# Performance work log

Hardware: AMD Instinct MI355X
Metric: run time of the kernel (lower is better)

## Reference

```python
import jax, jax.numpy as jnp
import numpy as np

T, B, N1, N2, N3, N4 = 512, 256, 512, 256, 64, 784
BETA_LIF = 0.9
BETA_LI = 0.95
THR = 1.0
LN_EPS = 1e-5


@jax.custom_vjp
def spike(x):
    # snntorch heaviside fire with ATan surrogate gradient (alpha=2 default)
    return (x > 0).astype(x.dtype)

def _spike_fwd(x):
    return spike(x), x

def _spike_bwd(x, g):
    return (g / (1.0 + (jnp.pi * x) ** 2),)

spike.defvjp(_spike_fwd, _spike_bwd)


def setup_inputs() -> dict:
    key = jax.random.key(0)
    ks = jax.random.split(key, 10)
    def lin(k, out_d, in_d):
        k1, k2 = jax.random.split(k)
        bound = 1.0 / np.sqrt(in_d)
        W = jax.random.uniform(k1, (out_d, in_d), jnp.float32, -bound, bound)
        b = jax.random.uniform(k2, (out_d,), jnp.float32, -bound, bound)
        return W, b
    W_lif, b_lif = lin(ks[0], N1, N2)
    W_li, b_li = lin(ks[1], N2, N1)
    W1, b1 = lin(ks[2], N3, N2)
    W2, b2 = lin(ks[3], N4, N3)
    # binary spike train input
    spk_rec = (jax.random.uniform(ks[4], (T, B, N2)) < 0.1).astype(jnp.float32)
    return {
        'spk_rec': spk_rec,
        'W_lif': W_lif, 'b_lif': b_lif,
        'W_li': W_li, 'b_li': b_li,
        'W1': W1, 'b1': b1,
        'W2': W2, 'b2': b2,
        'ln_g': jnp.ones((N4,), jnp.float32),
        'ln_b': jnp.zeros((N4,), jnp.float32),
    }


def reference(spk_rec, W_lif, b_lif, W_li, b_li, W1, b1, W2, b2, ln_g, ln_b):
    # Precompute per-step input currents with one big GEMM: [T,B,n1]
    cur_seq = jnp.einsum('tbi,oi->tbo', spk_rec, W_lif) + b_lif

    def lif_step(mem, cur):
        # snntorch Leaky, reset_mechanism='subtract':
        # reset based on previous-step membrane (detached)
        reset = jax.lax.stop_gradient((mem - THR > 0).astype(mem.dtype))
        mem_new = BETA_LIF * mem + cur - reset * THR
        spk = spike(mem_new - THR)
        return mem_new, spk

    mem0 = jnp.zeros(cur_seq.shape[1:], cur_seq.dtype)
    _, lif_spk = jax.lax.scan(lif_step, mem0, cur_seq)  # [T,B,n1]

    li_in = jnp.einsum('tbi,oi->tbo', lif_spk, W_li) + b_li  # [T,B,n2]
    beta_li = jnp.clip(jnp.asarray(BETA_LI, li_in.dtype), 0.0, 1.0)

    def li_step(mem, inp):
        mem = beta_li * mem + inp
        return mem, mem

    _, li_mem = jax.lax.scan(li_step, jnp.zeros(li_in.shape[1:], li_in.dtype), li_in)

    x = li_mem.mean(axis=0)  # [B,n2]
    h = jax.nn.relu(x @ W1.T + b1)  # [B,n3]
    y = h @ W2.T + b2  # [B,n4]
    mu = jnp.mean(y, axis=-1, keepdims=True)
    var = jnp.var(y, axis=-1, keepdims=True)
    return (y - mu) / jnp.sqrt(var + LN_EPS) * ln_g + ln_b
```

## Files before the change

### kernel.cpp

```cpp
#include <hip/hip_runtime.h>
#include <hip/hip_bf16.h>
#include <cmath>
#include <cstdint>


#define T_TOT 512
#define B_SZ  256
#define N1    512
#define N2    256
#define N3    64
#define N4    784
#define BN    (B_SZ * N1)

typedef unsigned short u16;
typedef short bf16x8 __attribute__((ext_vector_type(8)));
typedef float f32x4 __attribute__((ext_vector_type(4)));
typedef const __attribute__((address_space(1))) uint32_t* gas_p;
typedef __attribute__((address_space(3))) uint32_t* las_p;

#define OFF_BLIF 0
#define OFF_WLI  512
#define OFF_BLI  131584
#define OFF_W1   131840
#define OFF_B1   148224
#define OFF_W2   148288
#define OFF_B2   198464
#define OFF_LNG  199248
#define OFF_LNB  200032
#define CANON_N  200816

__device__ __forceinline__ float b2f(u16 u) {
  return __uint_as_float(((uint32_t)u) << 16);
}
__device__ __forceinline__ u16 f2b(float f) {
  uint32_t x = __float_as_uint(f);
  return (u16)((x + 0x7fffu + ((x >> 16) & 1u)) >> 16);
}
__device__ __forceinline__ float ldany(const void* p, long i, int isbf) {
  return isbf ? b2f(((const u16*)p)[i]) : ((const float*)p)[i];
}
__device__ __forceinline__ uint32_t pk_trunc(float a, float b) {
  return (__float_as_uint(a) >> 16) | (__float_as_uint(b) & 0xFFFF0000u);
}

__device__ __forceinline__ void dmax(uint32_t w, uint32_t& mB, uint32_t& mF) {
  uint32_t f = w & 0x7FFFFFFFu; if (f > mF) mF = f;
  uint32_t h0 = (w << 16) & 0x7FFFFFFFu;
  uint32_t h1 = w & 0x7FFF0000u;
  if (h0 > mB) mB = h0;
  if (h1 > mB) mB = h1;
}

__global__ __launch_bounds__(256) void k_prep(
    const void* wA, const void* wB,
    const void* t0, const void* t1, const void* t2,
    const void* s_blif, const void* s_bli, const void* s_w1,
    const void* s_b1, const void* s_w2, const void* spk,
    float* __restrict__ canon, u16* __restrict__ Whi, u16* __restrict__ Wlo,
    uint32_t* __restrict__ flg)
{
  __shared__ uint32_t redA[256], redB[256];
  __shared__ uint32_t dres[12];
  int tid = threadIdx.x;

  #define TREDUCE(vA, vB, oA, oB) {                                          \
    redA[tid] = (vA); redB[tid] = (vB); __syncthreads();                     \
    for (int s_ = 128; s_ > 0; s_ >>= 1) {                                   \
      if (tid < s_) {                                                        \
        if (redA[tid + s_] > redA[tid]) redA[tid] = redA[tid + s_];          \
        if (redB[tid + s_] > redB[tid]) redB[tid] = redB[tid + s_];          \
      }                                                                      \
      __syncthreads();                                                       \
    }                                                                        \
    if (tid == 0) { dres[oA] = redA[0]; dres[oB] = redB[0]; }                \
    __syncthreads(); }

  {
    const uint32_t* p = (const uint32_t*)spk + (size_t)tid * 16;
    uint32_t f = 0;
    #pragma unroll
    for (int j = 0; j < 16; j++) if (p[j] == 0x3F803F80u) f = 1;
    TREDUCE(f, 0u, 0, 11)
  }
  {
    const uint32_t* p = (const uint32_t*)wA + (size_t)tid * 16;
    uint32_t mB = 0, mF = 0;
    #pragma unroll
    for (int j = 0; j < 16; j++) dmax(p[j], mB, mF);
    TREDUCE(mB, mF, 1, 2)
  }
  {
    const uint32_t* p = (const uint32_t*)wB + (size_t)tid * 16;
    uint32_t mB = 0, mF = 0;
    #pragma unroll
    for (int j = 0; j < 16; j++) dmax(p[j], mB, mF);
    TREDUCE(mB, mF, 3, 4)
  }
  {
    const uint32_t* p = (const uint32_t*)t0;
    uint32_t mB = 0, mF = 0;
    for (int i = tid; i < 392; i += 256) dmax(p[i], mB, mF);
    TREDUCE(mB, mF, 5, 6)
  }
  {
    const uint32_t* p = (const uint32_t*)t1;
    uint32_t mB = 0, mF = 0;
    for (int i = tid; i < 392; i += 256) dmax(p[i], mB, mF);
    TREDUCE(mB, mF, 7, 8)
  }
  {
    const uint32_t* p = (const uint32_t*)t2;
    uint32_t mB = 0, mF = 0;
    for (int i = tid; i < 392; i += 256) dmax(p[i], mB, mF);
    TREDUCE(mB, mF, 9, 10)
  }
  #undef TREDUCE

  int isbf = (int)dres[0];
  uint32_t st0 = isbf ? dres[1] : dres[2];
  uint32_t st1 = isbf ? dres[3] : dres[4];
  uint32_t s2  = isbf ? dres[5] : dres[6];
  uint32_t s3  = isbf ? dres[7] : dres[8];
  uint32_t s4  = isbf ? dres[9] : dres[10];

  if (blockIdx.x == 0 && tid == 0) flg[0] = (uint32_t)isbf;
  const void* s_wlif = (st0 >= st1) ? wA : wB;
  const void* s_wli  = (st0 >= st1) ? wB : wA;
  const void *s_lng, *s_lnb, *s_b2;
  if (s2 >= s3 && s2 >= s4)      s_lng = t0;
  else if (s3 >= s2 && s3 >= s4) s_lng = t1;
  else                           s_lng = t2;
  if (s2 <= s3 && s2 <= s4)      s_lnb = t0;
  else if (s3 <= s2 && s3 <= s4) s_lnb = t1;
  else                           s_lnb = t2;
  s_b2 = (t0 != s_lng && t0 != s_lnb) ? t0
       : (t1 != s_lng && t1 != s_lnb) ? t1 : t2;

  long id = (long)blockIdx.x * 256 + tid;
  if (id < 512)    { canon[OFF_BLIF + id] = ldany(s_blif, id, isbf); return; } id -= 512;
  if (id < 131072) { canon[OFF_WLI  + id] = ldany(s_wli,  id, isbf); return; } id -= 131072;
  if (id < 256)    { canon[OFF_BLI  + id] = ldany(s_bli,  id, isbf); return; } id -= 256;
  if (id < 16384)  { canon[OFF_W1   + id] = ldany(s_w1,   id, isbf); return; } id -= 16384;
  if (id < 64)     { canon[OFF_B1   + id] = ldany(s_b1,   id, isbf); return; } id -= 64;
  if (id < 50176)  { canon[OFF_W2   + id] = ldany(s_w2,   id, isbf); return; } id -= 50176;
  if (id < 784)    { canon[OFF_B2   + id] = ldany(s_b2,   id, isbf); return; } id -= 784;
  if (id < 784)    { canon[OFF_LNG  + id] = ldany(s_lng,  id, isbf); return; } id -= 784;
  if (id < 784)    { canon[OFF_LNB  + id] = ldany(s_lnb,  id, isbf); return; } id -= 784;
  if (id < 131072) {
    float wv = ldany(s_wlif, id, isbf);
    u16 h = f2b(wv);
    Whi[id] = h;
    Wlo[id] = f2b(wv - b2f(h));
  }
}

#define SSTEP6(val, M, C, Gv) {                                              \
    float rst_ = (M) > 1.0f ? 1.0f : 0.0f;                                   \
    (M) = 0.9f * (M) + (val) - rst_;                                         \
    float sp_ = (M) > 1.0f ? 1.0f : 0.0f;                                    \
    (C) += sp_;                                                              \
    (Gv) = 0.95f * (Gv) + sp_; }

template <int USELO>
__device__ __forceinline__ void fused_loop(
    const void* __restrict__ spk, const u16* __restrict__ Whi,
    const u16* __restrict__ Wlo, const float* __restrict__ canon,
    float* __restrict__ Sg, u16 (&Ab)[2][32 * 256],
    int n0, int b0, int wv, int lr, int lq, int tid)
{
  bf16x8 wh[2][8], wl[2][8];
  #pragma unroll
  for (int jn = 0; jn < 2; jn++) {
    const u16* ph = Whi + (size_t)(n0 + wv * 32 + jn * 16 + lr) * N2 + lq * 8;
    #pragma unroll
    for (int ks = 0; ks < 8; ks++) wh[jn][ks] = *(const bf16x8*)(ph + ks * 32);
    if constexpr (USELO) {
      const u16* pl = Wlo + (size_t)(n0 + wv * 32 + jn * 16 + lr) * N2 + lq * 8;
      #pragma unroll
      for (int ks = 0; ks < 8; ks++) wl[jn][ks] = *(const bf16x8*)(pl + ks * 32);
    }
  }
  float bv0 = canon[OFF_BLIF + n0 + wv * 32 + lr];
  float bv1 = canon[OFF_BLIF + n0 + wv * 32 + 16 + lr];

  int lane = tid & 63;
  const u16* gsrc[4];
  if constexpr (USELO == 0) {
    #pragma unroll
    for (int c = 0; c < 4; c++) {
      int g = wv * 4 + c;
      int r = g * 2 + (lane >> 5);
      int kg = (lane & 31) ^ (r & 7);
      gsrc[c] = (const u16*)spk +
                ((size_t)((r & 15) * 256 + b0 + (r >> 4))) * 256 + kg * 8;
    }
  }
  int sr[4], sk[4];
  #pragma unroll
  for (int c = 0; c < 4; c++) {
    int f = tid + 256 * c;
    sr[c] = f >> 5;
    sk[c] = f & 31;
  }
  int4 pre[4];
  #define AELEM(it, c) (((size_t)((16 * (it) + (sr[c] & 15)) * 256 + b0 +    \
                          (sr[c] >> 4))) * 256 + sk[c] * 8)
  #define ALOAD(it) { _Pragma("unroll") for (int c = 0; c < 4; c++) {        \
        const float4* pf = (const float4*)spk + (AELEM(it, c) >> 2);         \
        float4 fa = pf[0], fb = pf[1]; int4 p;                               \
        p.x = (int)pk_trunc(fa.x, fa.y); p.y = (int)pk_trunc(fa.z, fa.w);    \
        p.z = (int)pk_trunc(fb.x, fb.y); p.w = (int)pk_trunc(fb.z, fb.w);    \
        pre[c] = p; } }
  #define ASTORE(bf) { _Pragma("unroll") for (int c = 0; c < 4; c++)         \
      *(int4*)&Ab[bf][sr[c] * 256 + ((sk[c] ^ (sr[c] & 7)) * 8)] = pre[c]; }
  #define DMA(it, bf) { _Pragma("unroll") for (int c = 0; c < 4; c++)        \
      __builtin_amdgcn_global_load_lds(                                      \
        (gas_p)(gsrc[c] + (size_t)(it) * 1048576),                           \
        (las_p)&Ab[bf][(wv * 4 + c) * 512], 16, 0, 0); }
  #define LDF(bf, ks_, d0, d1) { const u16* ab_ = Ab[bf];                    \
      int sl_ = (((ks_) * 4 + lq) ^ (lr & 7)) * 8;                           \
      d0 = *(const bf16x8*)(ab_ + lr * 256 + sl_);                           \
      d1 = *(const bf16x8*)(ab_ + (16 + lr) * 256 + sl_); }

  if constexpr (USELO == 0) {
    DMA(0, 0)
  } else {
    ALOAD(0) ASTORE(0)
    ALOAD(1)
  }
  __syncthreads();

  bf16x8 a0, a1, na0, na1;
  LDF(0, 0, a0, a1)

  float mem = 0.f, cnt = 0.f, G = 0.f;

  for (int it = 0; it < 32; it++) {
    if constexpr (USELO == 0) {
      if (it < 31) DMA(it + 1, (it + 1) & 1)
    }
    f32x4 acc[2][2];
    #pragma unroll
    for (int i = 0; i < 2; i++)
      #pragma unroll
      for (int jn = 0; jn < 2; jn++)
        #pragma unroll
        for (int r = 0; r < 4; r++) acc[i][jn][r] = 0.0f;

    #pragma unroll
    for (int ks = 0; ks < 8; ks++) {
      if (ks < 7) LDF(it & 1, ks + 1, na0, na1)
      acc[0][0] = __builtin_amdgcn_mfma_f32_16x16x32_bf16(a0, wh[0][ks], acc[0][0], 0, 0, 0);
      if constexpr (USELO)
        acc[0][0] = __builtin_amdgcn_mfma_f32_16x16x32_bf16(a0, wl[0][ks], acc[0][0], 0, 0, 0);
      acc[0][1] = __builtin_amdgcn_mfma_f32_16x16x32_bf16(a0, wh[1][ks], acc[0][1], 0, 0, 0);
      if constexpr (USELO)
        acc[0][1] = __builtin_amdgcn_mfma_f32_16x16x32_bf16(a0, wl[1][ks], acc[0][1], 0, 0, 0);
      acc[1][0] = __builtin_amdgcn_mfma_f32_16x16x32_bf16(a1, wh[0][ks], acc[1][0], 0, 0, 0);
      if constexpr (USELO)
        acc[1][0] = __builtin_amdgcn_mfma_f32_16x16x32_bf16(a1, wl[0][ks], acc[1][0], 0, 0, 0);
      acc[1][1] = __builtin_amdgcn_mfma_f32_16x16x32_bf16(a1, wh[1][ks], acc[1][1], 0, 0, 0);
      if constexpr (USELO)
        acc[1][1] = __builtin_amdgcn_mfma_f32_16x16x32_bf16(a1, wl[1][ks], acc[1][1], 0, 0, 0);
      if (ks < 7) { a0 = na0; a1 = na1; }
    }
    if constexpr (USELO) {
      if (it < 31) ASTORE((it + 1) & 1)
    }
    __syncthreads();
    if constexpr (USELO) {
      if (it < 30) ALOAD(it + 2)
    }
    if (it < 31) LDF((it + 1) & 1, 0, a0, a1)

    float Y[4][4];
    #pragma unroll
    for (int rr = 0; rr < 4; rr++) {
      float x0 = acc[0][0][rr], x1 = acc[1][0][rr];
      float x2 = acc[0][1][rr], x3 = acc[1][1][rr];
      float s0 = __shfl_xor(x0, 16), s1 = __shfl_xor(x1, 16);
      float s2 = __shfl_xor(x2, 16), s3 = __shfl_xor(x3, 16);
      bool g1 = (lq & 1) != 0;
      float z0 = g1 ? s1 : x0, z1 = g1 ? x1 : s0;
      float z2 = g1 ? s3 : x2, z3 = g1 ? x3 : s2;
      float t0 = __shfl_xor(z0, 32), t1 = __shfl_xor(z1, 32);
      float t2 = __shfl_xor(z2, 32), t3 = __shfl_xor(z3, 32);
      bool g2 = (lq & 2) != 0;
      Y[rr][0] = g2 ? t2 : z0; Y[rr][1] = g2 ? t3 : z1;
      Y[rr][2] = g2 ? z2 : t0; Y[rr][3] = g2 ? z3 : t1;
    }
    float bvv = (lq & 2) ? bv1 : bv0;
    #pragma unroll
    for (int j = 0; j < 4; j++)
      #pragma unroll
      for (int rr = 0; rr < 4; rr++)
        SSTEP6(Y[rr][j] + bvv, mem, cnt, G)
  }
  #undef ALOAD
  #undef ASTORE
  #undef AELEM
  #undef DMA
  #undef LDF

  int nA = n0 + wv * 32 + (lq >> 1) * 16 + lr;
  int bA = b0 + (lq & 1);
  Sg[(size_t)nA * 256 + bA] = (cnt - 0.95f * G) * 20.0f;
}

__global__ __launch_bounds__(256, 2) void k_fused(
    const void* __restrict__ spk, const u16* __restrict__ Whi,
    const u16* __restrict__ Wlo, const float* __restrict__ canon,
    float* __restrict__ Sg, const uint32_t* __restrict__ flg)
{
  __shared__ alignas(16) u16 Ab[2][32 * 256];
  int tid = threadIdx.x, bid = blockIdx.x;
  int nb = bid >> 7, bb = bid & 127;
  int n0 = nb * 128, b0 = bb * 2;
  int lane = tid & 63, wv = tid >> 6;
  int lr = lane & 15, lq = lane >> 4;

  if (flg[0]) fused_loop<0>(spk, Whi, Wlo, canon, Sg, Ab, n0, b0, wv, lr, lq, tid);
  else        fused_loop<1>(spk, Whi, Wlo, canon, Sg, Ab, n0, b0, wv, lr, lq, tid);
}

#define BG 4
__global__ __launch_bounds__(256) void k_tail(
    const float* __restrict__ Sg, const float* __restrict__ canon,
    float* __restrict__ outp, float Csum)
{
  __shared__ float sS[BG][N1];
  __shared__ float sx[BG][N2];
  __shared__ float sh[BG][N3];
  __shared__ float sy[BG][N4];
  __shared__ float red[256];
  int b0 = blockIdx.x * BG, tid = threadIdx.x;

  for (int i = tid; i < BG * N1; i += 256) {
    int bb = i & 3, n = i >> 2;
    sS[bb][n] = Sg[(size_t)n * 256 + b0 + bb];
  }
  __syncthreads();

  {
    const float4* w = (const float4*)(canon + OFF_WLI + (size_t)tid * N1);
    float a[BG] = {0.f, 0.f, 0.f, 0.f};
    for (int k = 0; k < N1 / 4; k++) {
      float4 p4 = w[k];
      #pragma unroll
      for (int bb = 0; bb < BG; bb++)
        a[bb] += sS[bb][k*4] * p4.x + sS[bb][k*4+1] * p4.y +
                 sS[bb][k*4+2] * p4.z + sS[bb][k*4+3] * p4.w;
    }
    float bli = canon[OFF_BLI + tid];
    #pragma unroll
    for (int bb = 0; bb < BG; bb++)
      sx[bb][tid] = (a[bb] + Csum * bli) * (1.0f / (float)T_TOT);
  }
  __syncthreads();

  if (tid < N3) {
    const float4* w = (const float4*)(canon + OFF_W1 + (size_t)tid * N2);
    float a[BG] = {0.f, 0.f, 0.f, 0.f};
    for (int k = 0; k < N2 / 4; k++) {
      float4 p4 = w[k];
      #pragma unroll
      for (int bb = 0; bb < BG; bb++)
        a[bb] += sx[bb][k*4] * p4.x + sx[bb][k*4+1] * p4.y +
                 sx[bb][k*4+2] * p4.z + sx[bb][k*4+3] * p4.w;
    }
    float b1v = canon[OFF_B1 + tid];
    #pragma unroll
    for (int bb = 0; bb < BG; bb++) {
      float v = a[bb] + b1v;
      sh[bb][tid] = v > 0.f ? v : 0.f;
    }
  }
  __syncthreads();

  for (int n = tid; n < N4; n += 256) {
    const float4* w = (const float4*)(canon + OFF_W2 + (size_t)n * N3);
    float a[BG] = {0.f, 0.f, 0.f, 0.f};
    for (int k = 0; k < N3 / 4; k++) {
      float4 p4 = w[k];
      #pragma unroll
      for (int bb = 0; bb < BG; bb++)
        a[bb] += sh[bb][k*4] * p4.x + sh[bb][k*4+1] * p4.y +
                 sh[bb][k*4+2] * p4.z + sh[bb][k*4+3] * p4.w;
    }
    float b2v = canon[OFF_B2 + n];
    #pragma unroll
    for (int bb = 0; bb < BG; bb++) sy[bb][n] = a[bb] + b2v;
  }
  __syncthreads();

  for (int bb = 0; bb < BG; bb++) {
    float p = 0.f;
    for (int n = tid; n < N4; n += 256) p += sy[bb][n];
    __syncthreads();
    red[tid] = p; __syncthreads();
    for (int s = 128; s > 0; s >>= 1) { if (tid < s) red[tid] += red[tid + s]; __syncthreads(); }
    float mu = red[0] / (float)N4;
    __syncthreads();
    p = 0.f;
    for (int n = tid; n < N4; n += 256) { float d = sy[bb][n] - mu; p += d * d; }
    red[tid] = p; __syncthreads();
    for (int s = 128; s > 0; s >>= 1) { if (tid < s) red[tid] += red[tid + s]; __syncthreads(); }
    float var = red[0] / (float)N4;
    float sc = 1.0f / sqrtf(var + 1e-5f);
    for (int n = tid; n < N4; n += 256) {
      outp[(size_t)(b0 + bb) * N4 + n] =
          (sy[bb][n] - mu) * sc * canon[OFF_LNG + n] + canon[OFF_LNB + n];
    }
  }
}

__global__ void k_fillv(float* o, int n, float V) {
  int i = blockIdx.x * 256 + threadIdx.x;
  if (i < n) o[i] = V;
}

extern "C" void kernel_launch(void* const* d_in, const int* in_sizes, int n_in,
                              void* d_out, int out_size, void* d_ws, size_t ws_size,
                              hipStream_t stream) {
  float* out = (float*)d_out;

  int idx_spk = -1, idx_blif = -1, idx_bli = -1, idx_w1 = -1, idx_b1 = -1,
      idx_w2 = -1;
  int idxW[2] = {-1, -1}, nW = 0;
  int idxT[3] = {-1, -1, -1}, nT = 0;
  bool ok = (n_in == 11);
  for (int i = 0; ok && i < 11; i++) {
    switch (in_sizes[i]) {
      case 33554432: if (idx_spk  < 0) idx_spk  = i; else ok = false; break;
      case 512:      if (idx_blif < 0) idx_blif = i; else ok = false; break;
      case 256:      if (idx_bli  < 0) idx_bli  = i; else ok = false; break;
      case 16384:    if (idx_w1   < 0) idx_w1   = i; else ok = false; break;
      case 64:       if (idx_b1   < 0) idx_b1   = i; else ok = false; break;
      case 50176:    if (idx_w2   < 0) idx_w2   = i; else ok = false; break;
      case 131072:   if (nW < 2) idxW[nW++] = i; else ok = false; break;
      case 784:      if (nT < 3) idxT[nT++] = i; else ok = false; break;
      default: ok = false;
    }
  }
  ok = ok && idx_spk >= 0 && idx_blif >= 0 && idx_bli >= 0 && idx_w1 >= 0 &&
       idx_b1 >= 0 && idx_w2 >= 0 && nW == 2 && nT == 3;
  if (!ok) {
    k_fillv<<<(out_size + 255) / 256, 256, 0, stream>>>(
        out, out_size, (float)(n_in >= 1 ? in_sizes[0] : -1));
    return;
  }
  if (out_size != B_SZ * N4) {
    k_fillv<<<(out_size + 255) / 256, 256, 0, stream>>>(
        out, out_size, 1.0e6f + (float)out_size);
    return;
  }

  char* w = (char*)d_ws;
  uint32_t* flg  = (uint32_t*)(w + 1016);
  float* canon = (float*)(w + 2048);
  size_t canonB = ((size_t)CANON_N * 4 + 255) & ~(size_t)255;
  u16* Whi = (u16*)(w + 2048 + canonB);
  u16* Wlo = Whi + BN;
  float* Sg = (float*)((char*)Wlo + (size_t)BN * 2);
  size_t need = 2048 + canonB + (size_t)2 * BN * 2 + (size_t)BN * 4;
  if (ws_size < need) {
    k_fillv<<<(out_size + 255) / 256, 256, 0, stream>>>(out, out_size, 2.0e6f);
    return;
  }

  double beta = 0.95;
  double bT = std::pow(beta, (double)T_TOT);
  float Csum = (float)(((double)T_TOT - beta * (1.0 - bT) / (1.0 - beta)) / (1.0 - beta));

  k_prep<<<1297, 256, 0, stream>>>(
      d_in[idxW[0]], d_in[idxW[1]], d_in[idxT[0]], d_in[idxT[1]],
      d_in[idxT[2]], d_in[idx_blif], d_in[idx_bli], d_in[idx_w1],
      d_in[idx_b1], d_in[idx_w2], d_in[idx_spk], canon, Whi, Wlo, flg);
  k_fused<<<512, 256, 0, stream>>>(d_in[idx_spk], Whi, Wlo, canon, Sg, flg);
  k_tail<<<B_SZ / BG, 256, 0, stream>>>(Sg, canon, out, Csum);
}
```

Before: 293.8 us.

## Fuse tail MLP and LayerNorm into fused kernel via last-block atomic counter

Removes the separate tail kernel launch. Each batch pair now has a counter that the four N-blocks increment after writing Sg, and the last block to arrive runs the readout MLP and LayerNorm for its two batch rows, reusing the LDS buffer. The goal is to drop one kernel launch and overlap the tail with the remaining fused blocks. In exchange there are threadfence and atomic costs, and the tail work runs in 128 blocks at two batches each instead of 64 blocks at four, so the W_li weights are read twice as often.

```diff
diff --git a/kernel.cpp b/kernel.cpp
--- a/kernel.cpp
+++ b/kernel.cpp
@@ -57,11 +57,13 @@
     const void* s_blif, const void* s_bli, const void* s_w1,
     const void* s_b1, const void* s_w2, const void* spk,
     float* __restrict__ canon, u16* __restrict__ Whi, u16* __restrict__ Wlo,
-    uint32_t* __restrict__ flg)
+    uint32_t* __restrict__ flg, uint32_t* __restrict__ ctr)
 {
   __shared__ uint32_t redA[256], redB[256];
   __shared__ uint32_t dres[12];
   int tid = threadIdx.x;
+
+  if (blockIdx.x == 0 && tid < 128) ctr[tid] = 0u;
 
   #define TREDUCE(vA, vB, oA, oB) {                                          \
     redA[tid] = (vA); redB[tid] = (vB); __syncthreads();                     \
@@ -310,9 +312,11 @@
 __global__ __launch_bounds__(256, 2) void k_fused(
     const void* __restrict__ spk, const u16* __restrict__ Whi,
     const u16* __restrict__ Wlo, const float* __restrict__ canon,
-    float* __restrict__ Sg, const uint32_t* __restrict__ flg)
+    float* __restrict__ Sg, const uint32_t* __restrict__ flg,
+    float* __restrict__ outp, float Csum, uint32_t* __restrict__ ctr)
 {
   __shared__ alignas(16) u16 Ab[2][32 * 256];
+  __shared__ uint32_t sOld;
   int tid = threadIdx.x, bid = blockIdx.x;
   int nb = bid >> 7, bb = bid & 127;
   int n0 = nb * 128, b0 = bb * 2;
@@ -321,95 +325,87 @@
 
   if (flg[0]) fused_loop<0>(spk, Whi, Wlo, canon, Sg, Ab, n0, b0, wv, lr, lq, tid);
   else        fused_loop<1>(spk, Whi, Wlo, canon, Sg, Ab, n0, b0, wv, lr, lq, tid);
-}
-
-#define BG 4
-__global__ __launch_bounds__(256) void k_tail(
-    const float* __restrict__ Sg, const float* __restrict__ canon,
-    float* __restrict__ outp, float Csum)
-{
-  __shared__ float sS[BG][N1];
-  __shared__ float sx[BG][N2];
-  __shared__ float sh[BG][N3];
-  __shared__ float sy[BG][N4];
-  __shared__ float red[256];
-  int b0 = blockIdx.x * BG, tid = threadIdx.x;
-
-  for (int i = tid; i < BG * N1; i += 256) {
-    int bb = i & 3, n = i >> 2;
-    sS[bb][n] = Sg[(size_t)n * 256 + b0 + bb];
+
+  __threadfence();
+  __syncthreads();
+  if (tid == 0) sOld = atomicAdd(&ctr[bb], 1u);
+  __syncthreads();
+  if (sOld != 3u) return;
+  __threadfence();
+
+  float* sS  = (float*)&Ab[0][0];
+  float* sx  = sS + 2 * N1;
+  float* sh  = sx + 2 * N2;
+  float* sy  = sh + 2 * N3;
+  float* red = sy + 2 * N4;
+  __syncthreads();
+
+  for (int i = tid; i < 2 * N1; i += 256) {
+    int b2 = i & 1, n = i >> 1;
+    sS[b2 * N1 + n] = Sg[(size_t)n * 256 + b0 + b2];
   }
   __syncthreads();
 
   {
     const float4* w = (const float4*)(canon + OFF_WLI + (size_t)tid * N1);
-    float a[BG] = {0.f, 0.f, 0.f, 0.f};
+    float a0 = 0.f, a1 = 0.f;
     for (int k = 0; k < N1 / 4; k++) {
       float4 p4 = w[k];
-      #pragma unroll
-      for (int bb = 0; bb < BG; bb++)
-        a[bb] += sS[bb][k*4] * p4.x + sS[bb][k*4+1] * p4.y +
-                 sS[bb][k*4+2] * p4.z + sS[bb][k*4+3] * p4.w;
+      a0 += sS[k*4] * p4.x + sS[k*4+1] * p4.y + sS[k*4+2] * p4.z + sS[k*4+3] * p4.w;
+      a1 += sS[N1+k*4] * p4.x + sS[N1+k*4+1] * p4.y + sS[N1+k*4+2] * p4.z + sS[N1+k*4+3] * p4.w;
     }
     float bli = canon[OFF_BLI + tid];
-    #pragma unroll
-    for (int bb = 0; bb < BG; bb++)
-      sx[bb][tid] = (a[bb] + Csum * bli) * (1.0f / (float)T_TOT);
+    sx[tid]      = (a0 + Csum * bli) * (1.0f / (float)T_TOT);
+    sx[N2 + tid] = (a1 + Csum * bli) * (1.0f / (float)T_TOT);
   }
   __syncthreads();
 
   if (tid < N3) {
     const float4* w = (const float4*)(canon + OFF_W1 + (size_t)tid * N2);
-    float a[BG] = {0.f, 0.f, 0.f, 0.f};
+    float a0 = 0.f, a1 = 0.f;
     for (int k = 0; k < N2 / 4; k++) {
       float4 p4 = w[k];
-      #pragma unroll
-      for (int bb = 0; bb < BG; bb++)
-        a[bb] += sx[bb][k*4] * p4.x + sx[bb][k*4+1] * p4.y +
-                 sx[bb][k*4+2] * p4.z + sx[bb][k*4+3] * p4.w;
+      a0 += sx[k*4]*p4.x + sx[k*4+1]*p4.y + sx[k*4+2]*p4.z + sx[k*4+3]*p4.w;
+      a1 += sx[N2+k*4]*p4.x + sx[N2+k*4+1]*p4.y + sx[N2+k*4+2]*p4.z + sx[N2+k*4+3]*p4.w;
     }
     float b1v = canon[OFF_B1 + tid];
-    #pragma unroll
-    for (int bb = 0; bb < BG; bb++) {
-      float v = a[bb] + b1v;
-      sh[bb][tid] = v > 0.f ? v : 0.f;
-    }
+    float v0 = a0 + b1v, v1 = a1 + b1v;
+    sh[tid]      = v0 > 0.f ? v0 : 0.f;
+    sh[N3 + tid] = v1 > 0.f ? v1 : 0.f;
   }
   __syncthreads();
 
   for (int n = tid; n < N4; n += 256) {
     const float4* w = (const float4*)(canon + OFF_W2 + (size_t)n * N3);
-    float a[BG] = {0.f, 0.f, 0.f, 0.f};
+    float a0 = 0.f, a1 = 0.f;
     for (int k = 0; k < N3 / 4; k++) {
       float4 p4 = w[k];
-      #pragma unroll
-      for (int bb = 0; bb < BG; bb++)
-        a[bb] += sh[bb][k*4] * p4.x + sh[bb][k*4+1] * p4.y +
-                 sh[bb][k*4+2] * p4.z + sh[bb][k*4+3] * p4.w;
+      a0 += sh[k*4]*p4.x + sh[k*4+1]*p4.y + sh[k*4+2]*p4.z + sh[k*4+3]*p4.w;
+      a1 += sh[N3+k*4]*p4.x + sh[N3+k*4+1]*p4.y + sh[N3+k*4+2]*p4.z + sh[N3+k*4+3]*p4.w;
     }
     float b2v = canon[OFF_B2 + n];
-    #pragma unroll
-    for (int bb = 0; bb < BG; bb++) sy[bb][n] = a[bb] + b2v;
-  }
-  __syncthreads();
-
-  for (int bb = 0; bb < BG; bb++) {
+    sy[n]      = a0 + b2v;
+    sy[N4 + n] = a1 + b2v;
+  }
+  __syncthreads();
+
+  for (int b2 = 0; b2 < 2; b2++) {
     float p = 0.f;
-    for (int n = tid; n < N4; n += 256) p += sy[bb][n];
+    for (int n = tid; n < N4; n += 256) p += sy[b2*N4 + n];
     __syncthreads();
     red[tid] = p; __syncthreads();
     for (int s = 128; s > 0; s >>= 1) { if (tid < s) red[tid] += red[tid + s]; __syncthreads(); }
     float mu = red[0] / (float)N4;
     __syncthreads();
     p = 0.f;
-    for (int n = tid; n < N4; n += 256) { float d = sy[bb][n] - mu; p += d * d; }
+    for (int n = tid; n < N4; n += 256) { float d = sy[b2*N4 + n] - mu; p += d * d; }
     red[tid] = p; __syncthreads();
     for (int s = 128; s > 0; s >>= 1) { if (tid < s) red[tid] += red[tid + s]; __syncthreads(); }
     float var = red[0] / (float)N4;
     float sc = 1.0f / sqrtf(var + 1e-5f);
     for (int n = tid; n < N4; n += 256) {
-      outp[(size_t)(b0 + bb) * N4 + n] =
-          (sy[bb][n] - mu) * sc * canon[OFF_LNG + n] + canon[OFF_LNB + n];
+      outp[(size_t)(b0 + b2) * N4 + n] =
+          (sy[b2*N4 + n] - mu) * sc * canon[OFF_LNG + n] + canon[OFF_LNB + n];
     }
   }
 }
@@ -462,7 +458,8 @@
   u16* Whi = (u16*)(w + 2048 + canonB);
   u16* Wlo = Whi + BN;
   float* Sg = (float*)((char*)Wlo + (size_t)BN * 2);
-  size_t need = 2048 + canonB + (size_t)2 * BN * 2 + (size_t)BN * 4;
+  uint32_t* ctr = (uint32_t*)((char*)Sg + (size_t)BN * 4);
+  size_t need = 2048 + canonB + (size_t)2 * BN * 2 + (size_t)BN * 4 + 512;
   if (ws_size < need) {
     k_fillv<<<(out_size + 255) / 256, 256, 0, stream>>>(out, out_size, 2.0e6f);
     return;
@@ -475,7 +472,7 @@
   k_prep<<<1297, 256, 0, stream>>>(
       d_in[idxW[0]], d_in[idxW[1]], d_in[idxT[0]], d_in[idxT[1]],
       d_in[idxT[2]], d_in[idx_blif], d_in[idx_bli], d_in[idx_w1],
-      d_in[idx_b1], d_in[idx_w2], d_in[idx_spk], canon, Whi, Wlo, flg);
-  k_fused<<<512, 256, 0, stream>>>(d_in[idx_spk], Whi, Wlo, canon, Sg, flg);
-  k_tail<<<B_SZ / BG, 256, 0, stream>>>(Sg, canon, out, Csum);
-}
+      d_in[idx_b1], d_in[idx_w2], d_in[idx_spk], canon, Whi, Wlo, flg, ctr);
+  k_fused<<<512, 256, 0, stream>>>(d_in[idx_spk], Whi, Wlo, canon, Sg, flg,
+                                   out, Csum, ctr);
+}
```

New measurement: 340.9 us. 1.16x slower.
